# Kernel optimization log

Measured on AMD Instinct MI355X. Metric: run time of the kernel, lower is better.

## Reference

```python
import jax, jax.numpy as jnp
import numpy as np

N, B, T, S, E, R = 4, 8, 512, 512, 1024, 1024


def setup_inputs() -> dict:
    key = jax.random.key(0)
    k1, k2, k3, k4, k5 = jax.random.split(key, 5)
    return {
        "query": jax.random.normal(k1, (1, B, T, E), dtype=jnp.float32),
        "key_value_states": jax.random.normal(k2, (N, B, S, R), dtype=jnp.float32),
        "attention_mask": jax.random.normal(k3, (1, B, T, S), dtype=jnp.float32),
        "Wk": jax.random.normal(k4, (E, R), dtype=jnp.float32) * (1.0 / np.sqrt(R)),
        "bk": jax.random.normal(k5, (E,), dtype=jnp.float32) * 0.01,
    }


def reference(query, key_value_states, attention_mask, Wk, bk):
    # k_proj: [N,B,S,R] @ [R,E] + bias -> [N,B,S,E]
    key = jnp.einsum("nbsr,er->nbse", key_value_states, Wk) + bk
    # QK^T (no scaling), query broadcast over N: [N,B,T,S]
    scores = jnp.einsum("bte,nbse->nbts", query[0], key)
    scores = scores + attention_mask  # mask broadcast over N
    attn = jax.nn.softmax(scores, axis=-1)
    # weights @ raw key_value_states (NOT projected key): [N,B,T,R]
    out = jnp.einsum("nbts,nbsr->nbtr", attn, key_value_states)
    return out
```

## Files before the change

kernel.cpp:

```cpp
#include <hip/hip_runtime.h>

typedef unsigned short u16;
typedef unsigned int u32;
typedef unsigned long long u64;

typedef __bf16 bfrag __attribute__((ext_vector_type(8)));
typedef float f32x4 __attribute__((ext_vector_type(4)));

typedef __attribute__((address_space(1))) char* gas1_p;
typedef __attribute__((address_space(3))) char* las3_p;

#define DI __device__ __forceinline__

DI u16 f2bf(float f) {
  u32 u = __float_as_uint(f);
  u += 0x7FFFu + ((u >> 16) & 1u);
  return (u16)(u >> 16);
}
DI float bf2f(u16 h) { return __uint_as_float(((u32)h) << 16); }

DI void gload16(const void* g, void* l) {
  __builtin_amdgcn_global_load_lds((gas1_p)(u64)g, (las3_p)(u32)(u64)l, 16, 0, 0);
}

template <int N>
DI void waitvm() {
  if constexpr (N >= 12)     asm volatile("s_waitcnt vmcnt(12)" ::: "memory");
  else if constexpr (N == 8) asm volatile("s_waitcnt vmcnt(8)" ::: "memory");
  else if constexpr (N == 6) asm volatile("s_waitcnt vmcnt(6)" ::: "memory");
  else if constexpr (N == 4) asm volatile("s_waitcnt vmcnt(4)" ::: "memory");
  else if constexpr (N == 3) asm volatile("s_waitcnt vmcnt(3)" ::: "memory");
  else                       asm volatile("s_waitcnt vmcnt(0)" ::: "memory");
}

__global__ __launch_bounds__(256) void k_split4(const float4* __restrict__ in,
                                                uint2* __restrict__ hi,
                                                uint2* __restrict__ lo) {
  int i = blockIdx.x * 256 + threadIdx.x;
  float4 v = in[i];
  u16 h0 = f2bf(v.x), h1 = f2bf(v.y), h2 = f2bf(v.z), h3 = f2bf(v.w);
  u16 l0 = f2bf(v.x - bf2f(h0)), l1 = f2bf(v.y - bf2f(h1));
  u16 l2 = f2bf(v.z - bf2f(h2)), l3 = f2bf(v.w - bf2f(h3));
  hi[i] = make_uint2((u32)h0 | ((u32)h1 << 16), (u32)h2 | ((u32)h3 << 16));
  lo[i] = make_uint2((u32)l0 | ((u32)l1 << 16), (u32)l2 | ((u32)l3 << 16));
}

template <int WH, int WTH, int WTL>
__global__ __launch_bounds__(256) void k_trsplit64(const float* __restrict__ in,
                                                   u16* __restrict__ hi, u16* __restrict__ lo,
                                                   u16* __restrict__ thi, u16* __restrict__ tlo,
                                                   int rows, int cols) {
  __shared__ float tile[64][65];
  const u64 zoff = (u64)blockIdx.z * (u64)rows * (u64)cols;
  const int r0 = threadIdx.x >> 4;
  const int c4 = (threadIdx.x & 15) << 2;
  const float* src = in + zoff + (u64)(blockIdx.y * 64 + r0) * cols + blockIdx.x * 64 + c4;
#pragma unroll
  for (int p = 0; p < 4; ++p) {
    float4 v = *reinterpret_cast<const float4*>(src + (u64)(p * 16) * cols);
    tile[r0 + p * 16][c4 + 0] = v.x;
    tile[r0 + p * 16][c4 + 1] = v.y;
    tile[r0 + p * 16][c4 + 2] = v.z;
    tile[r0 + p * 16][c4 + 3] = v.w;
  }
  __syncthreads();
  if constexpr (WH) {
    const int rr = threadIdx.x >> 3;
    const int cc = (threadIdx.x & 7) << 3;
#pragma unroll
    for (int p = 0; p < 2; ++p) {
      const int r = rr + p * 32;
      u32 h[4], l[4];
#pragma unroll
      for (int j = 0; j < 4; ++j) {
        float a = tile[r][cc + 2 * j], b = tile[r][cc + 2 * j + 1];
        u16 ha = f2bf(a), hb = f2bf(b);
        h[j] = (u32)ha | ((u32)hb << 16);
        l[j] = (u32)f2bf(a - bf2f(ha)) | ((u32)f2bf(b - bf2f(hb)) << 16);
      }
      const u64 o = zoff + (u64)(blockIdx.y * 64 + r) * cols + blockIdx.x * 64 + cc;
      *reinterpret_cast<uint4*>(hi + o) = make_uint4(h[0], h[1], h[2], h[3]);
      *reinterpret_cast<uint4*>(lo + o) = make_uint4(l[0], l[1], l[2], l[3]);
    }
  }
  if constexpr (WTH) {
#pragma unroll
    for (int p = 0; p < 2; ++p) {
      const int id = threadIdx.x + p * 256;
      const int col = id >> 3;
      const int s8 = (id & 7) << 3;
      u32 h[4], l[4];
#pragma unroll
      for (int j = 0; j < 4; ++j) {
        float a = tile[s8 + 2 * j][col], b = tile[s8 + 2 * j + 1][col];
        u16 ha = f2bf(a), hb = f2bf(b);
        h[j] = (u32)ha | ((u32)hb << 16);
        if constexpr (WTL)
          l[j] = (u32)f2bf(a - bf2f(ha)) | ((u32)f2bf(b - bf2f(hb)) << 16);
      }
      const u64 o = zoff + (u64)(blockIdx.x * 64 + col) * rows + blockIdx.y * 64 + s8;
      *reinterpret_cast<uint4*>(thi + o) = make_uint4(h[0], h[1], h[2], h[3]);
      if constexpr (WTL)
        *reinterpret_cast<uint4*>(tlo + o) = make_uint4(l[0], l[1], l[2], l[3]);
    }
  }
}

template <int X3, int FM, int ADDMASK, int SPLITOUT>
__global__ __launch_bounds__(512) void k_gemm8(
    const u16* __restrict__ Ah, const u16* __restrict__ Al,
    const u16* __restrict__ Bh, const u16* __restrict__ Bl,
    float* __restrict__ Cf, u16* __restrict__ Chi, u16* __restrict__ Clo,
    const float* __restrict__ Mask,
    int K, int N, int mt, int nt,
    u64 aStride, int aMask, u64 bStride, u64 cStride) {
  constexpr int BM = FM * 32;
  constexpr int A_U16 = BM * 32;
  constexpr int B_U16 = 128 * 32;
  constexpr int AL0 = A_U16;
  constexpr int BH0 = A_U16 * (1 + X3);
  constexpr int BL0 = BH0 + B_U16;
  constexpr int TILE = (A_U16 + B_U16) * (1 + X3);
  constexpr int CA = FM / 4;
  constexpr int L = (CA + 1) * (1 + X3);
  __shared__ u16 lds[3 * TILE];

  const int tid = threadIdx.x, lane = tid & 63;
  const int wid = tid >> 6, wr = wid >> 2, wn = wid & 3;

  const int g = (blockIdx.x & 7) * (gridDim.x >> 3) + (blockIdx.x >> 3);
  const int z = g / (mt * nt);
  const int rem = g - z * (mt * nt);
  const int ty = rem / nt, tx = rem - ty * nt;

  const u64 aOff = (u64)(z & aMask) * aStride;
  const u64 bOff = (u64)z * bStride;
  const u16* gA = Ah + aOff + (u64)ty * (u32)BM * (u32)K;
  const u16* gB = Bh + bOff + (u64)tx * 128u * (u32)K;
  const u16* gAl = nullptr;
  const u16* gBl = nullptr;
  if constexpr (X3) {
    gAl = Al + aOff + (u64)ty * (u32)BM * (u32)K;
    gBl = Bl + bOff + (u64)tx * 128u * (u32)K;
  }

  u64 aG[CA];
  u32 aLo[CA];
#pragma unroll
  for (int i = 0; i < CA; ++i) {
    const int c = i * 512 + tid;
    const int row = c >> 2, ks = c & 3;
    aG[i] = (u64)row * (u32)K + (u32)((ks ^ ((row >> 1) & 3)) << 3);
    aLo[i] = c << 3;
  }
  const int rowb = tid >> 2, ksb = tid & 3;
  const u64 bG = (u64)rowb * (u32)K + (u32)((ksb ^ ((rowb >> 1) & 3)) << 3);
  const u32 bLo = tid << 3;

  f32x4 acc[FM][2];
#pragma unroll
  for (int m = 0; m < FM; ++m)
#pragma unroll
    for (int n = 0; n < 2; ++n) acc[m][n] = (f32x4){0.f, 0.f, 0.f, 0.f};

  auto STAGE = [&](int bufU, int k0) {
#pragma unroll
    for (int i = 0; i < CA; ++i) {
      gload16(gA + aG[i] + (u32)k0, &lds[bufU + aLo[i]]);
      if constexpr (X3) gload16(gAl + aG[i] + (u32)k0, &lds[bufU + AL0 + aLo[i]]);
    }
    gload16(gB + bG + (u32)k0, &lds[bufU + BH0 + bLo]);
    if constexpr (X3) gload16(gBl + bG + (u32)k0, &lds[bufU + BL0 + bLo]);
  };

  const int swz = (((lane >> 1) & 3) ^ (lane >> 4)) << 3;
  auto COMPUTE = [&](int bufU) {
    bfrag ah[FM], alr[FM], bh[2], blr[2];
#pragma unroll
    for (int m = 0; m < FM; ++m) {
      const int idx = bufU + (wr * (BM / 2) + m * 16 + (lane & 15)) * 32 + swz;
      ah[m] = *reinterpret_cast<const bfrag*>(&lds[idx]);
      if constexpr (X3) alr[m] = *reinterpret_cast<const bfrag*>(&lds[idx + AL0]);
    }
#pragma unroll
    for (int n = 0; n < 2; ++n) {
      const int idx = bufU + BH0 + (wn * 32 + n * 16 + (lane & 15)) * 32 + swz;
      bh[n] = *reinterpret_cast<const bfrag*>(&lds[idx]);
      if constexpr (X3) blr[n] = *reinterpret_cast<const bfrag*>(&lds[idx + B_U16]);
    }
    __builtin_amdgcn_s_setprio(1);
#pragma unroll
    for (int m = 0; m < FM; ++m)
#pragma unroll
      for (int n = 0; n < 2; ++n) {
        acc[m][n] = __builtin_amdgcn_mfma_f32_16x16x32_bf16(ah[m], bh[n], acc[m][n], 0, 0, 0);
        if constexpr (X3) {
          acc[m][n] = __builtin_amdgcn_mfma_f32_16x16x32_bf16(ah[m], blr[n], acc[m][n], 0, 0, 0);
          acc[m][n] = __builtin_amdgcn_mfma_f32_16x16x32_bf16(alr[m], bh[n], acc[m][n], 0, 0, 0);
        }
      }
    __builtin_amdgcn_s_setprio(0);
  };

  const int NT = K >> 5;
  STAGE(0, 0);
  STAGE(TILE, 32);
  STAGE(2 * TILE, 64);
  int buf = 0;
  for (int t = 0; t < NT; ++t) {
    const int w = NT - 1 - t;
    if (w >= 2)      waitvm<2 * L>();
    else if (w == 1) waitvm<L>();
    else             waitvm<0>();
    __builtin_amdgcn_s_barrier();
    __builtin_amdgcn_sched_barrier(0);
    COMPUTE(buf * TILE);
    __builtin_amdgcn_s_barrier();
    __builtin_amdgcn_sched_barrier(0);
    if (t + 3 < NT) STAGE(buf * TILE, (t + 3) << 5);
    buf = (buf == 2) ? 0 : buf + 1;
  }

  const u64 cOff = (u64)z * cStride;
  const u64 mOff = (u64)(z & aMask) * cStride;
  const int rB = ty * BM + wr * (BM / 2) + (lane >> 4) * 4;
  const int cB = tx * 128 + wn * 32 + (lane & 15);
#pragma unroll
  for (int m = 0; m < FM; ++m)
#pragma unroll
    for (int n = 0; n < 2; ++n)
#pragma unroll
      for (int j = 0; j < 4; ++j) {
        const int rr = rB + m * 16 + j, cc = cB + n * 16;
        const u64 ci = cOff + (u64)rr * (u32)N + (u32)cc;
        float v = acc[m][n][j];
        if constexpr (ADDMASK) v += Mask[mOff + (u64)rr * (u32)N + (u32)cc];
        if constexpr (SPLITOUT) {
          u16 h = f2bf(v);
          Chi[ci] = h;
          Clo[ci] = f2bf(v - bf2f(h));
        } else {
          Cf[ci] = v;
        }
      }
}

__global__ __launch_bounds__(256) void k_softmax(const float* __restrict__ sc,
                                                 u16* __restrict__ attn) {
  const int row = blockIdx.x * 4 + (threadIdx.x >> 6);
  const int lane = threadIdx.x & 63;
  const float* srow = sc + (u64)row * 512 + lane * 8;
  float4 s0 = *reinterpret_cast<const float4*>(srow);
  float4 s1 = *reinterpret_cast<const float4*>(srow + 4);
  float x[8] = {s0.x, s0.y, s0.z, s0.w, s1.x, s1.y, s1.z, s1.w};
  float mx = x[0];
#pragma unroll
  for (int j = 1; j < 8; ++j) mx = fmaxf(mx, x[j]);
#pragma unroll
  for (int off = 32; off > 0; off >>= 1) mx = fmaxf(mx, __shfl_xor(mx, off));
  float sum = 0.f;
#pragma unroll
  for (int j = 0; j < 8; ++j) {
    x[j] = __expf(x[j] - mx);
    sum += x[j];
  }
#pragma unroll
  for (int off = 32; off > 0; off >>= 1) sum += __shfl_xor(sum, off);
  const float inv = 1.f / sum;
  u32 o[4];
#pragma unroll
  for (int j = 0; j < 4; ++j) {
    u16 e0 = f2bf(x[2 * j] * inv), e1 = f2bf(x[2 * j + 1] * inv);
    o[j] = (u32)e0 | ((u32)e1 << 16);
  }
  *reinterpret_cast<uint4*>(attn + (u64)row * 512 + lane * 8) = make_uint4(o[0], o[1], o[2], o[3]);
}

extern "C" void kernel_launch(void* const* d_in, const int* in_sizes, int n_in,
                              void* d_out, int out_size, void* d_ws, size_t ws_size,
                              hipStream_t stream) {
  const float* q = (const float*)d_in[0];
  const float* kvs = (const float*)d_in[1];
  const float* mask = (const float*)d_in[2];
  const float* Wk = (const float*)d_in[3];
  float* out = (float*)d_out;

  char* w = (char*)d_ws;
  u16* q_hi = (u16*)(w + 0);
  u16* q_lo = (u16*)(w + 8388608);
  u16* attn = (u16*)(w + 0);
  u16* wkt_hi = (u16*)(w + 16777216);
  u16* wkt_lo = (u16*)(w + 18874368);
  u16* qp_hi = (u16*)(w + 20971520);
  u16* qp_lo = (u16*)(w + 29360128);
  u16* kv_hi = (u16*)(w + 37748736);
  u16* kv_lo = (u16*)(w + 71303168);
  u16* kvt_hi = (u16*)(w + 104857600);
  float* sc = (float*)(w + 138412032);

  k_split4<<<dim3(4096), dim3(256), 0, stream>>>((const float4*)q, (uint2*)q_hi, (uint2*)q_lo);
  k_trsplit64<0, 1, 1><<<dim3(16, 16, 1), dim3(256), 0, stream>>>(
      Wk, (u16*)nullptr, (u16*)nullptr, wkt_hi, wkt_lo, 1024, 1024);
  k_trsplit64<1, 1, 0><<<dim3(16, 8, 32), dim3(256), 0, stream>>>(
      kvs, kv_hi, kv_lo, kvt_hi, (u16*)nullptr, 512, 1024);
  k_gemm8<1, 4, 0, 1><<<dim3(256), dim3(512), 0, stream>>>(
      q_hi, q_lo, wkt_hi, wkt_lo, (float*)nullptr, qp_hi, qp_lo, (const float*)nullptr,
      1024, 1024, 32, 8, (u64)0, 0, (u64)0, (u64)0);
  k_gemm8<1, 8, 1, 0><<<dim3(256), dim3(512), 0, stream>>>(
      qp_hi, qp_lo, kv_hi, kv_lo, sc, (u16*)nullptr, (u16*)nullptr, mask,
      1024, 512, 2, 4, (u64)524288, 7, (u64)524288, (u64)262144);
  k_softmax<<<dim3(4096), dim3(256), 0, stream>>>(sc, attn);
  k_gemm8<0, 8, 0, 0><<<dim3(512), dim3(512), 0, stream>>>(
      attn, (u16*)nullptr, kvt_hi, (u16*)nullptr, out, (u16*)nullptr, (u16*)nullptr,
      (const float*)nullptr, 512, 1024, 2, 8, (u64)262144, 31, (u64)524288, (u64)524288);

  (void)in_sizes; (void)n_in; (void)out_size; (void)ws_size;
}
```

Measured before the change: 176.0 us.

## Replace triple-buffered 8-wave GEMM with double-buffered 4-wave templated tile GEMM

```diff
diff --git a/kernel.cpp b/kernel.cpp
--- a/kernel.cpp
+++ b/kernel.cpp
@@ -21,16 +21,6 @@
 
 DI void gload16(const void* g, void* l) {
   __builtin_amdgcn_global_load_lds((gas1_p)(u64)g, (las3_p)(u32)(u64)l, 16, 0, 0);
-}
-
-template <int N>
-DI void waitvm() {
-  if constexpr (N >= 12)     asm volatile("s_waitcnt vmcnt(12)" ::: "memory");
-  else if constexpr (N == 8) asm volatile("s_waitcnt vmcnt(8)" ::: "memory");
-  else if constexpr (N == 6) asm volatile("s_waitcnt vmcnt(6)" ::: "memory");
-  else if constexpr (N == 4) asm volatile("s_waitcnt vmcnt(4)" ::: "memory");
-  else if constexpr (N == 3) asm volatile("s_waitcnt vmcnt(3)" ::: "memory");
-  else                       asm volatile("s_waitcnt vmcnt(0)" ::: "memory");
 }
 
 __global__ __launch_bounds__(256) void k_split4(const float4* __restrict__ in,
@@ -106,27 +96,26 @@
   }
 }
 
-template <int X3, int FM, int ADDMASK, int SPLITOUT>
-__global__ __launch_bounds__(512) void k_gemm8(
+template <int X3, int FM, int FN, int WR, int WC, int ADDMASK, int SPLITOUT>
+__global__ __launch_bounds__(WR * WC * 64, 2) void k_gemm2(
     const u16* __restrict__ Ah, const u16* __restrict__ Al,
     const u16* __restrict__ Bh, const u16* __restrict__ Bl,
     float* __restrict__ Cf, u16* __restrict__ Chi, u16* __restrict__ Clo,
     const float* __restrict__ Mask,
     int K, int N, int mt, int nt,
     u64 aStride, int aMask, u64 bStride, u64 cStride) {
-  constexpr int BM = FM * 32;
-  constexpr int A_U16 = BM * 32;
-  constexpr int B_U16 = 128 * 32;
+  constexpr int BM = WR * FM * 16, BN = WC * FN * 16;
+  constexpr int NTHR = WR * WC * 64;
+  constexpr int A_U16 = BM * 32, B_U16 = BN * 32;
   constexpr int AL0 = A_U16;
   constexpr int BH0 = A_U16 * (1 + X3);
-  constexpr int BL0 = BH0 + B_U16;
   constexpr int TILE = (A_U16 + B_U16) * (1 + X3);
-  constexpr int CA = FM / 4;
-  constexpr int L = (CA + 1) * (1 + X3);
-  __shared__ u16 lds[3 * TILE];
+  constexpr int CA = BM * 4 / NTHR;
+  constexpr int CB = BN * 4 / NTHR;
+  __shared__ u16 lds[2 * TILE];
 
   const int tid = threadIdx.x, lane = tid & 63;
-  const int wid = tid >> 6, wr = wid >> 2, wn = wid & 3;
+  const int wid = tid >> 6, wr = wid / WC, wc = wid % WC;
 
   const int g = (blockIdx.x & 7) * (gridDim.x >> 3) + (blockIdx.x >> 3);
   const int z = g / (mt * nt);
@@ -136,32 +125,38 @@
   const u64 aOff = (u64)(z & aMask) * aStride;
   const u64 bOff = (u64)z * bStride;
   const u16* gA = Ah + aOff + (u64)ty * (u32)BM * (u32)K;
-  const u16* gB = Bh + bOff + (u64)tx * 128u * (u32)K;
+  const u16* gB = Bh + bOff + (u64)tx * (u32)BN * (u32)K;
   const u16* gAl = nullptr;
   const u16* gBl = nullptr;
   if constexpr (X3) {
     gAl = Al + aOff + (u64)ty * (u32)BM * (u32)K;
-    gBl = Bl + bOff + (u64)tx * 128u * (u32)K;
+    gBl = Bl + bOff + (u64)tx * (u32)BN * (u32)K;
   }
 
   u64 aG[CA];
   u32 aLo[CA];
 #pragma unroll
   for (int i = 0; i < CA; ++i) {
-    const int c = i * 512 + tid;
+    const int c = i * NTHR + tid;
     const int row = c >> 2, ks = c & 3;
     aG[i] = (u64)row * (u32)K + (u32)((ks ^ ((row >> 1) & 3)) << 3);
     aLo[i] = c << 3;
   }
-  const int rowb = tid >> 2, ksb = tid & 3;
-  const u64 bG = (u64)rowb * (u32)K + (u32)((ksb ^ ((rowb >> 1) & 3)) << 3);
-  const u32 bLo = tid << 3;
-
-  f32x4 acc[FM][2];
+  u64 bG[CB];
+  u32 bLo[CB];
+#pragma unroll
+  for (int i = 0; i < CB; ++i) {
+    const int c = i * NTHR + tid;
+    const int row = c >> 2, ks = c & 3;
+    bG[i] = (u64)row * (u32)K + (u32)((ks ^ ((row >> 1) & 3)) << 3);
+    bLo[i] = c << 3;
+  }
+
+  f32x4 acc[FM][FN];
 #pragma unroll
   for (int m = 0; m < FM; ++m)
 #pragma unroll
-    for (int n = 0; n < 2; ++n) acc[m][n] = (f32x4){0.f, 0.f, 0.f, 0.f};
+    for (int n = 0; n < FN; ++n) acc[m][n] = (f32x4){0.f, 0.f, 0.f, 0.f};
 
   auto STAGE = [&](int bufU, int k0) {
 #pragma unroll
@@ -169,66 +164,63 @@
       gload16(gA + aG[i] + (u32)k0, &lds[bufU + aLo[i]]);
       if constexpr (X3) gload16(gAl + aG[i] + (u32)k0, &lds[bufU + AL0 + aLo[i]]);
     }
-    gload16(gB + bG + (u32)k0, &lds[bufU + BH0 + bLo]);
-    if constexpr (X3) gload16(gBl + bG + (u32)k0, &lds[bufU + BL0 + bLo]);
+#pragma unroll
+    for (int i = 0; i < CB; ++i) {
+      gload16(gB + bG[i] + (u32)k0, &lds[bufU + BH0 + bLo[i]]);
+      if constexpr (X3) gload16(gBl + bG[i] + (u32)k0, &lds[bufU + BH0 + B_U16 + bLo[i]]);
+    }
   };
 
   const int swz = (((lane >> 1) & 3) ^ (lane >> 4)) << 3;
   auto COMPUTE = [&](int bufU) {
-    bfrag ah[FM], alr[FM], bh[2], blr[2];
+    bfrag ah[FM], alr[FM], bh[FN], blr[FN];
 #pragma unroll
     for (int m = 0; m < FM; ++m) {
-      const int idx = bufU + (wr * (BM / 2) + m * 16 + (lane & 15)) * 32 + swz;
+      const int idx = bufU + (wr * (FM * 16) + m * 16 + (lane & 15)) * 32 + swz;
       ah[m] = *reinterpret_cast<const bfrag*>(&lds[idx]);
       if constexpr (X3) alr[m] = *reinterpret_cast<const bfrag*>(&lds[idx + AL0]);
     }
 #pragma unroll
-    for (int n = 0; n < 2; ++n) {
-      const int idx = bufU + BH0 + (wn * 32 + n * 16 + (lane & 15)) * 32 + swz;
+    for (int n = 0; n < FN; ++n) {
+      const int idx = bufU + BH0 + (wc * (FN * 16) + n * 16 + (lane & 15)) * 32 + swz;
       bh[n] = *reinterpret_cast<const bfrag*>(&lds[idx]);
       if constexpr (X3) blr[n] = *reinterpret_cast<const bfrag*>(&lds[idx + B_U16]);
     }
-    __builtin_amdgcn_s_setprio(1);
 #pragma unroll
     for (int m = 0; m < FM; ++m)
 #pragma unroll
-      for (int n = 0; n < 2; ++n) {
+      for (int n = 0; n < FN; ++n) {
         acc[m][n] = __builtin_amdgcn_mfma_f32_16x16x32_bf16(ah[m], bh[n], acc[m][n], 0, 0, 0);
         if constexpr (X3) {
           acc[m][n] = __builtin_amdgcn_mfma_f32_16x16x32_bf16(ah[m], blr[n], acc[m][n], 0, 0, 0);
           acc[m][n] = __builtin_amdgcn_mfma_f32_16x16x32_bf16(alr[m], bh[n], acc[m][n], 0, 0, 0);
         }
       }
-    __builtin_amdgcn_s_setprio(0);
   };
 
   const int NT = K >> 5;
   STAGE(0, 0);
-  STAGE(TILE, 32);
-  STAGE(2 * TILE, 64);
+  asm volatile("s_waitcnt vmcnt(0)" ::: "memory");
+  __builtin_amdgcn_s_barrier();
   int buf = 0;
   for (int t = 0; t < NT; ++t) {
-    const int w = NT - 1 - t;
-    if (w >= 2)      waitvm<2 * L>();
-    else if (w == 1) waitvm<L>();
-    else             waitvm<0>();
-    __builtin_amdgcn_s_barrier();
-    __builtin_amdgcn_sched_barrier(0);
-    COMPUTE(buf * TILE);
-    __builtin_amdgcn_s_barrier();
-    __builtin_amdgcn_sched_barrier(0);
-    if (t + 3 < NT) STAGE(buf * TILE, (t + 3) << 5);
-    buf = (buf == 2) ? 0 : buf + 1;
+    if (t + 1 < NT) STAGE(TILE - buf, (t + 1) << 5);
+    COMPUTE(buf);
+    if (t + 1 < NT) {
+      asm volatile("s_waitcnt vmcnt(0)" ::: "memory");
+      __builtin_amdgcn_s_barrier();
+      buf = TILE - buf;
+    }
   }
 
   const u64 cOff = (u64)z * cStride;
   const u64 mOff = (u64)(z & aMask) * cStride;
-  const int rB = ty * BM + wr * (BM / 2) + (lane >> 4) * 4;
-  const int cB = tx * 128 + wn * 32 + (lane & 15);
+  const int rB = ty * BM + wr * (FM * 16) + (lane >> 4) * 4;
+  const int cB = tx * BN + wc * (FN * 16) + (lane & 15);
 #pragma unroll
   for (int m = 0; m < FM; ++m)
 #pragma unroll
-    for (int n = 0; n < 2; ++n)
+    for (int n = 0; n < FN; ++n)
 #pragma unroll
       for (int j = 0; j < 4; ++j) {
         const int rr = rB + m * 16 + j, cc = cB + n * 16;
@@ -303,14 +295,14 @@
       Wk, (u16*)nullptr, (u16*)nullptr, wkt_hi, wkt_lo, 1024, 1024);
   k_trsplit64<1, 1, 0><<<dim3(16, 8, 32), dim3(256), 0, stream>>>(
       kvs, kv_hi, kv_lo, kvt_hi, (u16*)nullptr, 512, 1024);
-  k_gemm8<1, 4, 0, 1><<<dim3(256), dim3(512), 0, stream>>>(
+  k_gemm2<1, 4, 4, 2, 2, 0, 1><<<dim3(256), dim3(256), 0, stream>>>(
       q_hi, q_lo, wkt_hi, wkt_lo, (float*)nullptr, qp_hi, qp_lo, (const float*)nullptr,
       1024, 1024, 32, 8, (u64)0, 0, (u64)0, (u64)0);
-  k_gemm8<1, 8, 1, 0><<<dim3(256), dim3(512), 0, stream>>>(
+  k_gemm2<1, 4, 4, 2, 2, 1, 0><<<dim3(512), dim3(256), 0, stream>>>(
       qp_hi, qp_lo, kv_hi, kv_lo, sc, (u16*)nullptr, (u16*)nullptr, mask,
-      1024, 512, 2, 4, (u64)524288, 7, (u64)524288, (u64)262144);
+      1024, 512, 4, 4, (u64)524288, 7, (u64)524288, (u64)262144);
   k_softmax<<<dim3(4096), dim3(256), 0, stream>>>(sc, attn);
-  k_gemm8<0, 8, 0, 0><<<dim3(512), dim3(512), 0, stream>>>(
+  k_gemm2<0, 8, 4, 2, 2, 0, 0><<<dim3(512), dim3(256), 0, stream>>>(
       attn, (u16*)nullptr, kvt_hi, (u16*)nullptr, out, (u16*)nullptr, (u16*)nullptr,
       (const float*)nullptr, 512, 1024, 2, 8, (u64)262144, 31, (u64)524288, (u64)524288);
 
```

Measured after the change: 174.0 us. About the same (-1.2%).
